# Kernel tuning notes

Hardware: AMD Instinct MI355X
Metric: run time of the kernel (lower is better)

Reference implementation:

```python
import math
import jax, jax.numpy as jnp
import numpy as np

THETA = 10000.0

def _rope_rotate(x, pos):
    # x: [N,H,T,d] with d even; pos: [T] (int or float positions)
    d = x.shape[-1]
    freqs = THETA ** (-jnp.arange(0, d, 2, dtype=jnp.float32) / d)      # [d/2]
    ang = pos.astype(jnp.float32)[:, None] * freqs                       # [T, d/2]
    cos, sin = jnp.cos(ang), jnp.sin(ang)                                # broadcast over N,H
    x1, x2 = x[..., 0::2], x[..., 1::2]                                  # interleaved pairs
    r1 = x1 * cos - x2 * sin
    r2 = x1 * sin + x2 * cos
    return jnp.stack([r1, r2], axis=-1).reshape(x.shape)

def _apply_rope_2d(q, k, pos_h, pos_w):
    # axial 2D RoPE: first half of head_dim rotated by pos_h, second half by pos_w
    dh = q.shape[-1]
    half = dh // 2
    q = jnp.concatenate([_rope_rotate(q[..., :half], pos_h),
                         _rope_rotate(q[..., half:], pos_w)], axis=-1)
    k = jnp.concatenate([_rope_rotate(k[..., :half], pos_h),
                         _rope_rotate(k[..., half:], pos_w)], axis=-1)
    return q, k

def setup_inputs() -> dict:
    key = jax.random.key(0)
    ks = jax.random.split(key, 6)
    N, T, D, H = 4, 2048, 512, 8
    GH, GW = 64, 32  # 64x32 token grid, GH*GW == T
    x = jax.random.normal(ks[0], (N, T, D), dtype=jnp.float32)
    idx = jnp.arange(T, dtype=jnp.int32)
    pos_h = idx // GW
    pos_w = idx % GW
    scale_in = 1.0 / math.sqrt(D)
    w_qkv = jax.random.normal(ks[1], (D, 3 * D), dtype=jnp.float32) * scale_in
    w_proj = jax.random.normal(ks[2], (D, D), dtype=jnp.float32) * scale_in
    b_proj = jnp.zeros((D,), dtype=jnp.float32)
    return {"x": x, "pos_h": pos_h, "pos_w": pos_w,
            "w_qkv": w_qkv, "w_proj": w_proj, "b_proj": b_proj}

def reference(x, pos_h, pos_w, w_qkv, w_proj, b_proj):
    N, T, D = x.shape
    H = 8
    Dh = D // H
    qkv = x @ w_qkv                                   # [N,T,3D]
    q, k, v = jnp.split(qkv, 3, axis=-1)
    def to_heads(t):
        return t.reshape(N, T, H, Dh).transpose(0, 2, 1, 3)  # [N,H,T,Dh]
    q, k, v = to_heads(q), to_heads(k), to_heads(v)
    q, k = _apply_rope_2d(q, k, pos_h, pos_w)
    attn = jnp.einsum('nhtd,nhsd->nhts', q, k) * (1.0 / math.sqrt(Dh))  # [N,H,T,T]
    p = jax.nn.softmax(attn, axis=-1)
    o = jnp.einsum('nhts,nhsd->nhtd', p, v)           # [N,H,T,Dh]
    o = o.transpose(0, 2, 1, 3).reshape(N, T, D)
    return o @ w_proj + b_proj
```

## Files before the change

kernel.cpp:

```cpp
#include <hip/hip_runtime.h>

typedef __attribute__((ext_vector_type(4))) float f32x4;
typedef __attribute__((ext_vector_type(8))) _Float16 f16x8;
typedef __attribute__((ext_vector_type(2))) __fp16 fp16x2_raw;
typedef __attribute__((ext_vector_type(4))) unsigned int u32x4;
typedef __attribute__((ext_vector_type(2))) unsigned int u32x2;

#define MFMA_F16(a, b, c) __builtin_amdgcn_mfma_f32_16x16x32_f16((a), (b), (c), 0, 0, 0)

__device__ __forceinline__ unsigned int pkrtz(float a, float b) {
  union { fp16x2_raw h; unsigned int u; } v;
  v.h = __builtin_amdgcn_cvt_pkrtz(a, b);
  return v.u;
}

__device__ __forceinline__ float fexp2(float x) {
#if __has_builtin(__builtin_amdgcn_exp2f)
  return __builtin_amdgcn_exp2f(x);
#else
  float r;
  asm("v_exp_f32 %0, %1" : "=v"(r) : "v"(x));
  return r;
#endif
}

typedef const __attribute__((address_space(1))) unsigned int ga_u32_t;
typedef __attribute__((address_space(3))) unsigned int ls_u32_t;
__device__ __forceinline__ void gload16(const void* g, void* l) {
  __builtin_amdgcn_global_load_lds((ga_u32_t*)g, (ls_u32_t*)l, 16, 0, 0);
}

__global__ __launch_bounds__(256)
void k_prep_w(const float* __restrict__ in, _Float16* __restrict__ out, int N) {
  __shared__ float t[64][65];
  const int tid = threadIdx.x;
  const int bn = blockIdx.x * 64, bk = blockIdx.y * 64;
  #pragma unroll
  for (int it = 0; it < 16; ++it) {
    int idx = it * 256 + tid;
    int kk = idx >> 6, nn = idx & 63;
    t[kk][nn] = in[(bk + kk) * N + bn + nn];
  }
  __syncthreads();
  #pragma unroll
  for (int it = 0; it < 16; ++it) {
    int idx = it * 256 + tid;
    int nn = idx >> 6, kk = idx & 63;
    out[(bn + nn) * 512 + bk + kk] = (_Float16)t[kk][nn];
  }
}

__global__ __launch_bounds__(256, 3)
void k_gemm_qkv(const float* __restrict__ x,
                const _Float16* __restrict__ wT,
                const int* __restrict__ pos_h,
                const int* __restrict__ pos_w,
                _Float16* __restrict__ qh,
                _Float16* __restrict__ kh,
                _Float16* __restrict__ vT) {
  __shared__ char As[8192], Bs[8192];
  const int tid = threadIdx.x;
  const int lane = tid & 63, w = tid >> 6;
  const int lr = lane & 15, g = lane >> 4;
  const int m0 = blockIdx.y * 128;
  const int n0 = blockIdx.x * 128;
  const int wr = w >> 1, wc = w & 1;

  f32x4 acc[4][4];
  #pragma unroll
  for (int i = 0; i < 4; ++i)
    #pragma unroll
    for (int j = 0; j < 4; ++j) acc[i][j] = (f32x4){0.f, 0.f, 0.f, 0.f};

  for (int kt = 0; kt < 16; ++kt) {
    const int k0 = kt * 32;
    __syncthreads();
    #pragma unroll
    for (int it = 0; it < 2; ++it) {
      int idx = it * 256 + tid;
      int r = idx >> 2, ch = idx & 3;
      const float* px = x + (size_t)(m0 + r) * 512 + k0 + ch * 8;
      f32x4 v0 = *(const f32x4*)px;
      f32x4 v1 = *(const f32x4*)(px + 4);
      u32x4 d;
      d.x = pkrtz(v0[0], v0[1]); d.y = pkrtz(v0[2], v0[3]);
      d.z = pkrtz(v1[0], v1[1]); d.w = pkrtz(v1[2], v1[3]);
      *(u32x4*)(As + (((r << 6) + (ch << 4)) ^ ((r & 7) << 4))) = d;
    }
    #pragma unroll
    for (int it = 0; it < 2; ++it) {
      int idx = it * 256 + tid;
      int r = idx >> 2, ch = idx & 3;
      u32x4 d = *(const u32x4*)(wT + (n0 + r) * 512 + k0 + ch * 8);
      *(u32x4*)(Bs + (((r << 6) + (ch << 4)) ^ ((r & 7) << 4))) = d;
    }
    __syncthreads();

    f16x8 af[4], bf[4];
    #pragma unroll
    for (int mi = 0; mi < 4; ++mi) {
      int r = 64 * wr + 16 * mi + lr;
      af[mi] = *(const f16x8*)(As + (((r << 6) + (g << 4)) ^ ((r & 7) << 4)));
    }
    #pragma unroll
    for (int nj = 0; nj < 4; ++nj) {
      int r = 64 * wc + 16 * nj + lr;
      bf[nj] = *(const f16x8*)(Bs + (((r << 6) + (g << 4)) ^ ((r & 7) << 4)));
    }
    __builtin_amdgcn_s_setprio(1);
    #pragma unroll
    for (int mi = 0; mi < 4; ++mi)
      #pragma unroll
      for (int nj = 0; nj < 4; ++nj)
        acc[mi][nj] = MFMA_F16(af[mi], bf[nj], acc[mi][nj]);
    __builtin_amdgcn_s_setprio(0);
  }

  #pragma unroll
  for (int mi = 0; mi < 4; ++mi) {
    const int r0f = m0 + 64 * wr + 16 * mi + 4 * g;
    const int n = r0f >> 11;
    const int t = r0f & 2047;
    #pragma unroll
    for (int nj = 0; nj < 4; ++nj) {
      const int c = n0 + 64 * wc + 16 * nj + lr;
      const int mat = c >> 9;
      const int hh = (c >> 6) & 7;
      const int dh = c & 63;
      f32x4 v = acc[mi][nj];
      if (mat == 2) {
        int tperm = (t & ~31) + 8 * ((t >> 2) & 3) + 4 * ((t >> 4) & 1);
        u32x2 pk2;
        pk2.x = pkrtz(v[0], v[1]);
        pk2.y = pkrtz(v[2], v[3]);
        *(u32x2*)(vT + (size_t)((n * 8 + hh) * 64 + dh) * 2048 + tperm) = pk2;
      } else {
        const int p = (dh & 31) >> 1;
        const float freq = exp2f((float)p * -0.8304820237218405f);
        const int odd = lane & 1;
        const int* posArr = (dh < 32) ? pos_h : pos_w;
        _Float16* dst = mat ? kh : qh;
        const float scale = mat ? 1.0f : 0.125f * 1.44269504088896f;
        #pragma unroll
        for (int i = 0; i < 4; ++i) {
          float val = v[i];
          float oth = __shfl_xor(val, 1);
          float ang = (float)posArr[t + i] * freq;
          float sv, cv;
          __sincosf(ang, &sv, &cv);
          float x1 = odd ? oth : val;
          float x2 = odd ? val : oth;
          float res = odd ? (x1 * sv + x2 * cv) : (x1 * cv - x2 * sv);
          dst[(size_t)((n * 8 + hh) * 2048 + t + i) * 64 + dh] = (_Float16)(res * scale);
        }
      }
    }
  }
}

__global__ __launch_bounds__(256, 2)
void k_attn(const _Float16* __restrict__ qh,
            const _Float16* __restrict__ kh,
            const _Float16* __restrict__ vp,
            _Float16* __restrict__ o_flat) {
  __shared__ char Ks[2][16384];
  __shared__ char Vs[2][16384];
  const int tid = threadIdx.x, lane = tid & 63, w = tid >> 6;
  const int lr = lane & 15, g = lane >> 4;
  const int bid = blockIdx.x;
  const int qt = (bid >> 3) & 15;
  const int nh = (bid & 7) + 8 * (bid >> 7);

  f16x8 qf[2][2];
  const _Float16* qbase = qh + ((size_t)nh * 2048 + qt * 128 + w * 32) * 64;
  #pragma unroll
  for (int mi = 0; mi < 2; ++mi)
    #pragma unroll
    for (int kg = 0; kg < 2; ++kg)
      qf[mi][kg] = *(const f16x8*)(qbase + (16 * mi + lr) * 64 + kg * 32 + g * 8);

  f16x8 ones;
  #pragma unroll
  for (int i = 0; i < 8; ++i) ones[i] = (_Float16)1.0f;

  f32x4 oacc[2][4];
  f32x4 lacc4[2];
  #pragma unroll
  for (int mi = 0; mi < 2; ++mi) {
    lacc4[mi] = (f32x4){0.f, 0.f, 0.f, 0.f};
    #pragma unroll
    for (int nf = 0; nf < 4; ++nf) oacc[mi][nf] = (f32x4){0.f, 0.f, 0.f, 0.f};
  }

  const _Float16* kb = kh + (size_t)nh * 2048 * 64;
  const _Float16* vb = vp + (size_t)nh * 64 * 2048;

  const int rr = lane >> 3, cc = lane & 7;
  const _Float16* ksrc[2];
  const _Float16* vsrc[2];
  #pragma unroll
  for (int c = 0; c < 2; ++c) {
    int seg = w * 2 + c;
    int r = seg * 8 + rr;
    ksrc[c] = kb + (size_t)r * 64 + ((cc ^ (r & 7)) << 3);
    vsrc[c] = vb + (size_t)r * 2048 + ((cc ^ (r & 7)) << 3);
  }
  auto stage = [&](int b, int kt2) {
    #pragma unroll
    for (int h = 0; h < 2; ++h) {
      int kt = kt2 * 2 + h;
      #pragma unroll
      for (int c = 0; c < 2; ++c) {
        int seg = w * 2 + c;
        gload16(ksrc[c] + (size_t)kt * 4096, Ks[b] + h * 8192 + seg * 1024);
        gload16(vsrc[c] + (size_t)kt * 64,   Vs[b] + h * 8192 + seg * 1024);
      }
    }
  };

  stage(0, 0);

  const f32x4 cinit = (f32x4){-8.f, -8.f, -8.f, -8.f};

  for (int kt2 = 0; kt2 < 16; ++kt2) {
    const int cur = kt2 & 1;
    asm volatile("" ::: "memory");
    __builtin_amdgcn_s_barrier();
    if (kt2 + 1 < 16) {
      stage(cur ^ 1, kt2 + 1);
      asm volatile("s_waitcnt vmcnt(8)" ::: "memory");
    } else {
      asm volatile("s_waitcnt vmcnt(0)" ::: "memory");
    }
    __builtin_amdgcn_s_barrier();
    asm volatile("" ::: "memory");

    f32x4 sacc[2][2][4];
    #pragma unroll
    for (int h = 0; h < 2; ++h)
      #pragma unroll
      for (int mi = 0; mi < 2; ++mi)
        #pragma unroll
        for (int sj = 0; sj < 4; ++sj) sacc[h][mi][sj] = cinit;

    __builtin_amdgcn_s_setprio(1);
    #pragma unroll
    for (int h = 0; h < 2; ++h) {
      const char* Kb = Ks[cur] + h * 8192;
      #pragma unroll
      for (int sj = 0; sj < 4; ++sj) {
        int s = sj * 16 + lr;
        int rb = s << 7, sw = (s & 7) << 4;
        #pragma unroll
        for (int kg = 0; kg < 2; ++kg) {
          f16x8 kf = *(const f16x8*)(Kb + ((rb + (kg << 6) + (g << 4)) ^ sw));
          sacc[h][0][sj] = MFMA_F16(kf, qf[0][kg], sacc[h][0][sj]);
          sacc[h][1][sj] = MFMA_F16(kf, qf[1][kg], sacc[h][1][sj]);
        }
      }
    }
    __builtin_amdgcn_s_setprio(0);

    #pragma unroll
    for (int h = 0; h < 2; ++h) {
      const char* Vb = Vs[cur] + h * 8192;
      #pragma unroll
      for (int mi = 0; mi < 2; ++mi)
        #pragma unroll
        for (int sj = 0; sj < 4; ++sj) {
          sacc[h][mi][sj][0] = fexp2(sacc[h][mi][sj][0]);
          sacc[h][mi][sj][1] = fexp2(sacc[h][mi][sj][1]);
          sacc[h][mi][sj][2] = fexp2(sacc[h][mi][sj][2]);
          sacc[h][mi][sj][3] = fexp2(sacc[h][mi][sj][3]);
        }
      __builtin_amdgcn_s_setprio(1);
      #pragma unroll
      for (int t = 0; t < 2; ++t) {
        f16x8 vf[4];
        #pragma unroll
        for (int nf = 0; nf < 4; ++nf) {
          int dh = 16 * nf + lr;
          vf[nf] = *(const f16x8*)(Vb + (((dh << 7) + (t << 6) + (g << 4)) ^ ((dh & 7) << 4)));
        }
        #pragma unroll
        for (int mi = 0; mi < 2; ++mi) {
          union { unsigned int u[4]; f16x8 h; } pb;
          pb.u[0] = pkrtz(sacc[h][mi][2 * t][0], sacc[h][mi][2 * t][1]);
          pb.u[1] = pkrtz(sacc[h][mi][2 * t][2], sacc[h][mi][2 * t][3]);
          pb.u[2] = pkrtz(sacc[h][mi][2 * t + 1][0], sacc[h][mi][2 * t + 1][1]);
          pb.u[3] = pkrtz(sacc[h][mi][2 * t + 1][2], sacc[h][mi][2 * t + 1][3]);
          lacc4[mi] = MFMA_F16(ones, pb.h, lacc4[mi]);
          #pragma unroll
          for (int nf = 0; nf < 4; ++nf)
            oacc[mi][nf] = MFMA_F16(vf[nf], pb.h, oacc[mi][nf]);
        }
      }
      __builtin_amdgcn_s_setprio(0);
    }
  }

  const int n = nh >> 3, h2 = nh & 7;
  #pragma unroll
  for (int mi = 0; mi < 2; ++mi) {
    float inv = 1.0f / lacc4[mi][0];
    int row = qt * 128 + w * 32 + 16 * mi + lr;
    _Float16* orow = o_flat + ((size_t)(n * 2048 + row)) * 512 + h2 * 64;
    #pragma unroll
    for (int nf = 0; nf < 4; ++nf) {
      u32x2 pk2;
      pk2.x = pkrtz(oacc[mi][nf][0] * inv, oacc[mi][nf][1] * inv);
      pk2.y = pkrtz(oacc[mi][nf][2] * inv, oacc[mi][nf][3] * inv);
      *(u32x2*)(orow + 16 * nf + 4 * g) = pk2;
    }
  }
}

__global__ __launch_bounds__(256, 3)
void k_gemm_proj(const _Float16* __restrict__ o_flat,
                 const _Float16* __restrict__ wpT,
                 const float* __restrict__ bias,
                 float* __restrict__ out) {
  __shared__ char As[8192], Bs[8192];
  const int tid = threadIdx.x;
  const int lane = tid & 63, w = tid >> 6;
  const int lr = lane & 15, g = lane >> 4;
  const int m0 = blockIdx.y * 128;
  const int n0 = blockIdx.x * 128;
  const int wr = w >> 1, wc = w & 1;

  f32x4 acc[4][4];
  #pragma unroll
  for (int i = 0; i < 4; ++i)
    #pragma unroll
    for (int j = 0; j < 4; ++j) acc[i][j] = (f32x4){0.f, 0.f, 0.f, 0.f};

  for (int kt = 0; kt < 16; ++kt) {
    const int k0 = kt * 32;
    __syncthreads();
    #pragma unroll
    for (int it = 0; it < 2; ++it) {
      int idx = it * 256 + tid;
      int r = idx >> 2, ch = idx & 3;
      u32x4 d = *(const u32x4*)(o_flat + (m0 + r) * 512 + k0 + ch * 8);
      *(u32x4*)(As + (((r << 6) + (ch << 4)) ^ ((r & 7) << 4))) = d;
    }
    #pragma unroll
    for (int it = 0; it < 2; ++it) {
      int idx = it * 256 + tid;
      int r = idx >> 2, ch = idx & 3;
      u32x4 d = *(const u32x4*)(wpT + (n0 + r) * 512 + k0 + ch * 8);
      *(u32x4*)(Bs + (((r << 6) + (ch << 4)) ^ ((r & 7) << 4))) = d;
    }
    __syncthreads();

    f16x8 af[4], bf[4];
    #pragma unroll
    for (int mi = 0; mi < 4; ++mi) {
      int r = 64 * wr + 16 * mi + lr;
      af[mi] = *(const f16x8*)(As + (((r << 6) + (g << 4)) ^ ((r & 7) << 4)));
    }
    #pragma unroll
    for (int nj = 0; nj < 4; ++nj) {
      int r = 64 * wc + 16 * nj + lr;
      bf[nj] = *(const f16x8*)(Bs + (((r << 6) + (g << 4)) ^ ((r & 7) << 4)));
    }
    __builtin_amdgcn_s_setprio(1);
    #pragma unroll
    for (int mi = 0; mi < 4; ++mi)
      #pragma unroll
      for (int nj = 0; nj < 4; ++nj)
        acc[mi][nj] = MFMA_F16(af[mi], bf[nj], acc[mi][nj]);
    __builtin_amdgcn_s_setprio(0);
  }

  #pragma unroll
  for (int mi = 0; mi < 4; ++mi) {
    int r0f = m0 + 64 * wr + 16 * mi + 4 * g;
    #pragma unroll
    for (int nj = 0; nj < 4; ++nj) {
      int c = n0 + 64 * wc + 16 * nj + lr;
      float b = bias[c];
      #pragma unroll
      for (int i = 0; i < 4; ++i)
        out[(size_t)(r0f + i) * 512 + c] = acc[mi][nj][i] + b;
    }
  }
}

extern "C" void kernel_launch(void* const* d_in, const int* in_sizes, int n_in,
                              void* d_out, int out_size, void* d_ws, size_t ws_size,
                              hipStream_t stream) {
  const float* x      = (const float*)d_in[0];
  const int*   pos_h  = (const int*)d_in[1];
  const int*   pos_w  = (const int*)d_in[2];
  const float* w_qkv  = (const float*)d_in[3];
  const float* w_proj = (const float*)d_in[4];
  const float* b_proj = (const float*)d_in[5];
  float* out = (float*)d_out;

  char* ws = (char*)d_ws;
  size_t off = 0;
  auto alloc = [&](size_t bytes) {
    char* p = ws + off;
    off += (bytes + 1023) & ~(size_t)1023;
    return p;
  };
  _Float16* qh     = (_Float16*)alloc((size_t)32 * 2048 * 64 * 2);
  _Float16* kh     = (_Float16*)alloc((size_t)32 * 2048 * 64 * 2);
  _Float16* vT     = (_Float16*)alloc((size_t)32 * 2048 * 64 * 2);
  _Float16* o_flat = (_Float16*)alloc((size_t)8192 * 512 * 2);
  _Float16* wqT    = (_Float16*)alloc((size_t)1536 * 512 * 2);
  _Float16* wpT    = (_Float16*)alloc((size_t)512 * 512 * 2);

  hipLaunchKernelGGL(k_prep_w, dim3(24, 8), dim3(256), 0, stream, w_qkv, wqT, 1536);
  hipLaunchKernelGGL(k_prep_w, dim3(8, 8), dim3(256), 0, stream, w_proj, wpT, 512);
  hipLaunchKernelGGL(k_gemm_qkv, dim3(12, 64), dim3(256), 0, stream,
                     x, wqT, pos_h, pos_w, qh, kh, vT);
  hipLaunchKernelGGL(k_attn, dim3(512), dim3(256), 0, stream, qh, kh, vT, o_flat);
  hipLaunchKernelGGL(k_gemm_proj, dim3(4, 64), dim3(256), 0, stream, o_flat, wpT, b_proj, out);
}
```

Before: 95.92 us.

## Split attention waves across key halves and reduce partial outputs via LDS

```diff
diff --git a/kernel.cpp b/kernel.cpp
--- a/kernel.cpp
+++ b/kernel.cpp
@@ -167,14 +167,16 @@
   __shared__ char Vs[2][16384];
   const int tid = threadIdx.x, lane = tid & 63, w = tid >> 6;
   const int lr = lane & 15, g = lane >> 4;
+  const int qhlf = w >> 1;
+  const int shlf = w & 1;
   const int bid = blockIdx.x;
   const int qt = (bid >> 3) & 15;
   const int nh = (bid & 7) + 8 * (bid >> 7);
 
-  f16x8 qf[2][2];
-  const _Float16* qbase = qh + ((size_t)nh * 2048 + qt * 128 + w * 32) * 64;
-  #pragma unroll
-  for (int mi = 0; mi < 2; ++mi)
+  f16x8 qf[4][2];
+  const _Float16* qbase = qh + ((size_t)nh * 2048 + qt * 128 + qhlf * 64) * 64;
+  #pragma unroll
+  for (int mi = 0; mi < 4; ++mi)
     #pragma unroll
     for (int kg = 0; kg < 2; ++kg)
       qf[mi][kg] = *(const f16x8*)(qbase + (16 * mi + lr) * 64 + kg * 32 + g * 8);
@@ -183,10 +185,10 @@
   #pragma unroll
   for (int i = 0; i < 8; ++i) ones[i] = (_Float16)1.0f;
 
-  f32x4 oacc[2][4];
-  f32x4 lacc4[2];
-  #pragma unroll
-  for (int mi = 0; mi < 2; ++mi) {
+  f32x4 oacc[4][4];
+  f32x4 lacc4[4];
+  #pragma unroll
+  for (int mi = 0; mi < 4; ++mi) {
     lacc4[mi] = (f32x4){0.f, 0.f, 0.f, 0.f};
     #pragma unroll
     for (int nf = 0; nf < 4; ++nf) oacc[mi][nf] = (f32x4){0.f, 0.f, 0.f, 0.f};
@@ -235,82 +237,97 @@
     __builtin_amdgcn_s_barrier();
     asm volatile("" ::: "memory");
 
-    f32x4 sacc[2][2][4];
-    #pragma unroll
-    for (int h = 0; h < 2; ++h)
-      #pragma unroll
-      for (int mi = 0; mi < 2; ++mi)
+    const char* Kb = Ks[cur] + shlf * 8192;
+    const char* Vb = Vs[cur] + shlf * 8192;
+
+    f32x4 sacc[4][4];
+    #pragma unroll
+    for (int mi = 0; mi < 4; ++mi)
+      #pragma unroll
+      for (int sj = 0; sj < 4; ++sj) sacc[mi][sj] = cinit;
+
+    __builtin_amdgcn_s_setprio(1);
+    #pragma unroll
+    for (int sj = 0; sj < 4; ++sj) {
+      int s = sj * 16 + lr;
+      int rb = s << 7, sw = (s & 7) << 4;
+      #pragma unroll
+      for (int kg = 0; kg < 2; ++kg) {
+        f16x8 kf = *(const f16x8*)(Kb + ((rb + (kg << 6) + (g << 4)) ^ sw));
         #pragma unroll
-        for (int sj = 0; sj < 4; ++sj) sacc[h][mi][sj] = cinit;
+        for (int mi = 0; mi < 4; ++mi)
+          sacc[mi][sj] = MFMA_F16(kf, qf[mi][kg], sacc[mi][sj]);
+      }
+    }
+    __builtin_amdgcn_s_setprio(0);
+
+    #pragma unroll
+    for (int mi = 0; mi < 4; ++mi)
+      #pragma unroll
+      for (int sj = 0; sj < 4; ++sj) {
+        sacc[mi][sj][0] = fexp2(sacc[mi][sj][0]);
+        sacc[mi][sj][1] = fexp2(sacc[mi][sj][1]);
+        sacc[mi][sj][2] = fexp2(sacc[mi][sj][2]);
+        sacc[mi][sj][3] = fexp2(sacc[mi][sj][3]);
+      }
 
     __builtin_amdgcn_s_setprio(1);
     #pragma unroll
-    for (int h = 0; h < 2; ++h) {
-      const char* Kb = Ks[cur] + h * 8192;
-      #pragma unroll
-      for (int sj = 0; sj < 4; ++sj) {
-        int s = sj * 16 + lr;
-        int rb = s << 7, sw = (s & 7) << 4;
+    for (int t = 0; t < 2; ++t) {
+      f16x8 vf[4];
+      #pragma unroll
+      for (int nf = 0; nf < 4; ++nf) {
+        int dh = 16 * nf + lr;
+        vf[nf] = *(const f16x8*)(Vb + (((dh << 7) + (t << 6) + (g << 4)) ^ ((dh & 7) << 4)));
+      }
+      #pragma unroll
+      for (int mi = 0; mi < 4; ++mi) {
+        union { unsigned int u[4]; f16x8 h; } pb;
+        pb.u[0] = pkrtz(sacc[mi][2 * t][0], sacc[mi][2 * t][1]);
+        pb.u[1] = pkrtz(sacc[mi][2 * t][2], sacc[mi][2 * t][3]);
+        pb.u[2] = pkrtz(sacc[mi][2 * t + 1][0], sacc[mi][2 * t + 1][1]);
+        pb.u[3] = pkrtz(sacc[mi][2 * t + 1][2], sacc[mi][2 * t + 1][3]);
+        lacc4[mi] = MFMA_F16(ones, pb.h, lacc4[mi]);
         #pragma unroll
-        for (int kg = 0; kg < 2; ++kg) {
-          f16x8 kf = *(const f16x8*)(Kb + ((rb + (kg << 6) + (g << 4)) ^ sw));
-          sacc[h][0][sj] = MFMA_F16(kf, qf[0][kg], sacc[h][0][sj]);
-          sacc[h][1][sj] = MFMA_F16(kf, qf[1][kg], sacc[h][1][sj]);
-        }
+        for (int nf = 0; nf < 4; ++nf)
+          oacc[mi][nf] = MFMA_F16(vf[nf], pb.h, oacc[mi][nf]);
       }
     }
     __builtin_amdgcn_s_setprio(0);
-
-    #pragma unroll
-    for (int h = 0; h < 2; ++h) {
-      const char* Vb = Vs[cur] + h * 8192;
-      #pragma unroll
-      for (int mi = 0; mi < 2; ++mi)
-        #pragma unroll
-        for (int sj = 0; sj < 4; ++sj) {
-          sacc[h][mi][sj][0] = fexp2(sacc[h][mi][sj][0]);
-          sacc[h][mi][sj][1] = fexp2(sacc[h][mi][sj][1]);
-          sacc[h][mi][sj][2] = fexp2(sacc[h][mi][sj][2]);
-          sacc[h][mi][sj][3] = fexp2(sacc[h][mi][sj][3]);
-        }
-      __builtin_amdgcn_s_setprio(1);
-      #pragma unroll
-      for (int t = 0; t < 2; ++t) {
-        f16x8 vf[4];
-        #pragma unroll
-        for (int nf = 0; nf < 4; ++nf) {
-          int dh = 16 * nf + lr;
-          vf[nf] = *(const f16x8*)(Vb + (((dh << 7) + (t << 6) + (g << 4)) ^ ((dh & 7) << 4)));
-        }
-        #pragma unroll
-        for (int mi = 0; mi < 2; ++mi) {
-          union { unsigned int u[4]; f16x8 h; } pb;
-          pb.u[0] = pkrtz(sacc[h][mi][2 * t][0], sacc[h][mi][2 * t][1]);
-          pb.u[1] = pkrtz(sacc[h][mi][2 * t][2], sacc[h][mi][2 * t][3]);
-          pb.u[2] = pkrtz(sacc[h][mi][2 * t + 1][0], sacc[h][mi][2 * t + 1][1]);
-          pb.u[3] = pkrtz(sacc[h][mi][2 * t + 1][2], sacc[h][mi][2 * t + 1][3]);
-          lacc4[mi] = MFMA_F16(ones, pb.h, lacc4[mi]);
-          #pragma unroll
-          for (int nf = 0; nf < 4; ++nf)
-            oacc[mi][nf] = MFMA_F16(vf[nf], pb.h, oacc[mi][nf]);
-        }
-      }
-      __builtin_amdgcn_s_setprio(0);
-    }
-  }
-
-  const int n = nh >> 3, h2 = nh & 7;
-  #pragma unroll
-  for (int mi = 0; mi < 2; ++mi) {
-    float inv = 1.0f / lacc4[mi][0];
-    int row = qt * 128 + w * 32 + 16 * mi + lr;
-    _Float16* orow = o_flat + ((size_t)(n * 2048 + row)) * 512 + h2 * 64;
-    #pragma unroll
-    for (int nf = 0; nf < 4; ++nf) {
-      u32x2 pk2;
-      pk2.x = pkrtz(oacc[mi][nf][0] * inv, oacc[mi][nf][1] * inv);
-      pk2.y = pkrtz(oacc[mi][nf][2] * inv, oacc[mi][nf][3] * inv);
-      *(u32x2*)(orow + 16 * nf + 4 * g) = pk2;
+  }
+
+  __syncthreads();
+  float* obuf = (float*)(Ks[0]) + qhlf * 4096;
+  float* lbuf = (float*)(Vs[0]) + qhlf * 256;
+  if (shlf == 1) {
+    #pragma unroll
+    for (int mi = 0; mi < 4; ++mi)
+      #pragma unroll
+      for (int nf = 0; nf < 4; ++nf)
+        *(f32x4*)(obuf + ((mi * 4 + nf) * 64 + lane) * 4) = oacc[mi][nf];
+    f32x4 lv;
+    #pragma unroll
+    for (int mi = 0; mi < 4; ++mi) lv[mi] = lacc4[mi][0];
+    *(f32x4*)(lbuf + lane * 4) = lv;
+  }
+  __syncthreads();
+  if (shlf == 0) {
+    f32x4 lv = *(f32x4*)(lbuf + lane * 4);
+    const int n = nh >> 3, h2 = nh & 7;
+    #pragma unroll
+    for (int mi = 0; mi < 4; ++mi) {
+      float inv = 1.0f / (lacc4[mi][0] + lv[mi]);
+      int row = qt * 128 + qhlf * 64 + 16 * mi + lr;
+      _Float16* orow = o_flat + ((size_t)(n * 2048 + row)) * 512 + h2 * 64;
+      #pragma unroll
+      for (int nf = 0; nf < 4; ++nf) {
+        f32x4 part = *(f32x4*)(obuf + ((mi * 4 + nf) * 64 + lane) * 4);
+        f32x4 o = oacc[mi][nf] + part;
+        u32x2 pk2;
+        pk2.x = pkrtz(o[0] * inv, o[1] * inv);
+        pk2.y = pkrtz(o[2] * inv, o[3] * inv);
+        *(u32x2*)(orow + 16 * nf + 4 * g) = pk2;
+      }
     }
   }
 }
```

Result: no change. 96.62 us (+0.7%).

## Use direct global-to-LDS loads in GEMMs with pre-converted fp16 input

Applied to the files above, without the earlier changes.

```diff
diff --git a/kernel.cpp b/kernel.cpp
--- a/kernel.cpp
+++ b/kernel.cpp
@@ -23,11 +23,42 @@
   return r;
 #endif
 }
+__device__ __forceinline__ float fsin_rev(float x) {
+#if __has_builtin(__builtin_amdgcn_sinf)
+  return __builtin_amdgcn_sinf(x);
+#else
+  float r; asm("v_sin_f32 %0, %1" : "=v"(r) : "v"(x)); return r;
+#endif
+}
+__device__ __forceinline__ float fcos_rev(float x) {
+#if __has_builtin(__builtin_amdgcn_cosf)
+  return __builtin_amdgcn_cosf(x);
+#else
+  float r; asm("v_cos_f32 %0, %1" : "=v"(r) : "v"(x)); return r;
+#endif
+}
 
 typedef const __attribute__((address_space(1))) unsigned int ga_u32_t;
 typedef __attribute__((address_space(3))) unsigned int ls_u32_t;
 __device__ __forceinline__ void gload16(const void* g, void* l) {
   __builtin_amdgcn_global_load_lds((ga_u32_t*)g, (ls_u32_t*)l, 16, 0, 0);
+}
+
+__device__ __forceinline__ void inv_swz64(int seg, int lane, int& r, int& ch) {
+  int r_hi = seg * 8 + (lane >> 3);
+  int r0 = ((lane >> 2) & 1) ^ ((r_hi >> 1) & 1);
+  r = (r_hi << 1) | r0;
+  ch = (lane & 3) ^ (r & 3);
+}
+
+__global__ __launch_bounds__(256)
+void k_prep_x(const float* __restrict__ in, _Float16* __restrict__ out) {
+  int i = (blockIdx.x * 256 + threadIdx.x) * 4;
+  f32x4 v = *(const f32x4*)(in + i);
+  u32x2 p;
+  p.x = pkrtz(v[0], v[1]);
+  p.y = pkrtz(v[2], v[3]);
+  *(u32x2*)(out + i) = p;
 }
 
 __global__ __launch_bounds__(256)
@@ -51,7 +82,7 @@
 }
 
 __global__ __launch_bounds__(256, 3)
-void k_gemm_qkv(const float* __restrict__ x,
+void k_gemm_qkv(const _Float16* __restrict__ xh,
                 const _Float16* __restrict__ wT,
                 const int* __restrict__ pos_h,
                 const int* __restrict__ pos_w,
@@ -66,6 +97,16 @@
   const int n0 = blockIdx.x * 128;
   const int wr = w >> 1, wc = w & 1;
 
+  const _Float16* asrc[2];
+  const _Float16* bsrc[2];
+  #pragma unroll
+  for (int c = 0; c < 2; ++c) {
+    int seg = w * 2 + c, r, ch;
+    inv_swz64(seg, lane, r, ch);
+    asrc[c] = xh + (size_t)(m0 + r) * 512 + ch * 8;
+    bsrc[c] = wT + (size_t)(n0 + r) * 512 + ch * 8;
+  }
+
   f32x4 acc[4][4];
   #pragma unroll
   for (int i = 0; i < 4; ++i)
@@ -76,23 +117,9 @@
     const int k0 = kt * 32;
     __syncthreads();
     #pragma unroll
-    for (int it = 0; it < 2; ++it) {
-      int idx = it * 256 + tid;
-      int r = idx >> 2, ch = idx & 3;
-      const float* px = x + (size_t)(m0 + r) * 512 + k0 + ch * 8;
-      f32x4 v0 = *(const f32x4*)px;
-      f32x4 v1 = *(const f32x4*)(px + 4);
-      u32x4 d;
-      d.x = pkrtz(v0[0], v0[1]); d.y = pkrtz(v0[2], v0[3]);
-      d.z = pkrtz(v1[0], v1[1]); d.w = pkrtz(v1[2], v1[3]);
-      *(u32x4*)(As + (((r << 6) + (ch << 4)) ^ ((r & 7) << 4))) = d;
-    }
-    #pragma unroll
-    for (int it = 0; it < 2; ++it) {
-      int idx = it * 256 + tid;
-      int r = idx >> 2, ch = idx & 3;
-      u32x4 d = *(const u32x4*)(wT + (n0 + r) * 512 + k0 + ch * 8);
-      *(u32x4*)(Bs + (((r << 6) + (ch << 4)) ^ ((r & 7) << 4))) = d;
+    for (int c = 0; c < 2; ++c) {
+      gload16(asrc[c] + k0, As + (w * 2 + c) * 1024);
+      gload16(bsrc[c] + k0, Bs + (w * 2 + c) * 1024);
     }
     __syncthreads();
 
@@ -136,7 +163,7 @@
         *(u32x2*)(vT + (size_t)((n * 8 + hh) * 64 + dh) * 2048 + tperm) = pk2;
       } else {
         const int p = (dh & 31) >> 1;
-        const float freq = exp2f((float)p * -0.8304820237218405f);
+        const float freq_rev = fexp2((float)p * -0.8304820237218405f) * 0.15915494309189535f;
         const int odd = lane & 1;
         const int* posArr = (dh < 32) ? pos_h : pos_w;
         _Float16* dst = mat ? kh : qh;
@@ -145,9 +172,10 @@
         for (int i = 0; i < 4; ++i) {
           float val = v[i];
           float oth = __shfl_xor(val, 1);
-          float ang = (float)posArr[t + i] * freq;
-          float sv, cv;
-          __sincosf(ang, &sv, &cv);
+          float ar = (float)posArr[t + i] * freq_rev;
+          ar = ar - floorf(ar);
+          float sv = fsin_rev(ar);
+          float cv = fcos_rev(ar);
           float x1 = odd ? oth : val;
           float x2 = odd ? val : oth;
           float res = odd ? (x1 * sv + x2 * cv) : (x1 * cv - x2 * sv);
@@ -328,6 +356,16 @@
   const int n0 = blockIdx.x * 128;
   const int wr = w >> 1, wc = w & 1;
 
+  const _Float16* asrc[2];
+  const _Float16* bsrc[2];
+  #pragma unroll
+  for (int c = 0; c < 2; ++c) {
+    int seg = w * 2 + c, r, ch;
+    inv_swz64(seg, lane, r, ch);
+    asrc[c] = o_flat + (size_t)(m0 + r) * 512 + ch * 8;
+    bsrc[c] = wpT + (size_t)(n0 + r) * 512 + ch * 8;
+  }
+
   f32x4 acc[4][4];
   #pragma unroll
   for (int i = 0; i < 4; ++i)
@@ -338,18 +376,9 @@
     const int k0 = kt * 32;
     __syncthreads();
     #pragma unroll
-    for (int it = 0; it < 2; ++it) {
-      int idx = it * 256 + tid;
-      int r = idx >> 2, ch = idx & 3;
-      u32x4 d = *(const u32x4*)(o_flat + (m0 + r) * 512 + k0 + ch * 8);
-      *(u32x4*)(As + (((r << 6) + (ch << 4)) ^ ((r & 7) << 4))) = d;
-    }
-    #pragma unroll
-    for (int it = 0; it < 2; ++it) {
-      int idx = it * 256 + tid;
-      int r = idx >> 2, ch = idx & 3;
-      u32x4 d = *(const u32x4*)(wpT + (n0 + r) * 512 + k0 + ch * 8);
-      *(u32x4*)(Bs + (((r << 6) + (ch << 4)) ^ ((r & 7) << 4))) = d;
+    for (int c = 0; c < 2; ++c) {
+      gload16(asrc[c] + k0, As + (w * 2 + c) * 1024);
+      gload16(bsrc[c] + k0, Bs + (w * 2 + c) * 1024);
     }
     __syncthreads();
 
@@ -405,6 +434,7 @@
     off += (bytes + 1023) & ~(size_t)1023;
     return p;
   };
+  _Float16* xh     = (_Float16*)alloc((size_t)8192 * 512 * 2);
   _Float16* qh     = (_Float16*)alloc((size_t)32 * 2048 * 64 * 2);
   _Float16* kh     = (_Float16*)alloc((size_t)32 * 2048 * 64 * 2);
   _Float16* vT     = (_Float16*)alloc((size_t)32 * 2048 * 64 * 2);
@@ -412,10 +442,11 @@
   _Float16* wqT    = (_Float16*)alloc((size_t)1536 * 512 * 2);
   _Float16* wpT    = (_Float16*)alloc((size_t)512 * 512 * 2);
 
+  hipLaunchKernelGGL(k_prep_x, dim3(4096), dim3(256), 0, stream, x, xh);
   hipLaunchKernelGGL(k_prep_w, dim3(24, 8), dim3(256), 0, stream, w_qkv, wqT, 1536);
   hipLaunchKernelGGL(k_prep_w, dim3(8, 8), dim3(256), 0, stream, w_proj, wpT, 512);
   hipLaunchKernelGGL(k_gemm_qkv, dim3(12, 64), dim3(256), 0, stream,
-                     x, wqT, pos_h, pos_w, qh, kh, vT);
+                     xh, wqT, pos_h, pos_w, qh, kh, vT);
   hipLaunchKernelGGL(k_attn, dim3(512), dim3(256), 0, stream, qh, kh, vT, o_flat);
   hipLaunchKernelGGL(k_gemm_proj, dim3(4, 64), dim3(256), 0, stream, o_flat, wpT, b_proj, out);
 }
```

Result: faster. 92.98 us (-3.1%).
